# Kernel optimization log

Hardware: AMD Instinct MI355X
Metric: run time of the kernel (lower is better)

The kernel has to match this reference:

```python
import jax, jax.numpy as jnp
import numpy as np

TEMPERATURE = 0.5   # cfg.LOSS.TEMPERATURE
REG = 0.5           # Sinkhorn entropic regularization
NUM_ITER = 100      # numItermax in forward call
STOP_THR = 1e-9

BS, NUM_CLASSES, DIM = 16384, 1000, 512


def _l2norm(x):
    return x / jnp.linalg.norm(x, axis=-1, keepdims=True)


def setup_inputs() -> dict:
    key = jax.random.key(0)
    k1, k2, k3 = jax.random.split(key, 3)
    features = _l2norm(jax.random.normal(k1, (BS, DIM), jnp.float32))
    text_features = _l2norm(jax.random.normal(k2, (NUM_CLASSES, DIM), jnp.float32))
    ratios = jax.random.uniform(k3, (NUM_CLASSES,), jnp.float32)
    ratios = ratios / ratios.sum()  # class prior, sums to 1
    return {"features": features, "text_features": text_features, "ratios": ratios}


def sinkhorn_knopp(a, b, M, reg):
    """Faithful Sinkhorn-Knopp: u/v scaling loop with NaN/Inf bail-out and
    every-10-iters convergence check, unrolled as a masked lax.scan."""
    dim_a, dim_b = a.shape[0], b.shape[0]
    K = jnp.exp(M / -reg)                 # [dim_a, dim_b]
    Kp = (1.0 / a)[:, None] * K           # [dim_a, dim_b]
    u0 = jnp.ones((dim_a,), M.dtype) / dim_a
    v0 = jnp.ones((dim_b,), M.dtype) / dim_b

    def step(carry, ii):
        u, v, done = carry
        KtU = K.T @ u                     # [dim_b]
        v_new = b / KtU
        u_new = 1.0 / (Kp @ v_new)        # [dim_a]
        bad = (jnp.any(KtU == 0)
               | jnp.any(~jnp.isfinite(u_new))
               | jnp.any(~jnp.isfinite(v_new)))
        # err check (original does it when ii % 10 == 0)
        tmp2 = (u_new @ K) * v_new        # einsum('i,ij,j->j', u, K, v)
        err = jnp.linalg.norm(tmp2 - b)
        converged = ((ii % 10) == 0) & (err < STOP_THR)
        keep_prev = done | bad            # revert to uprev/vprev on bad, freeze after done
        u2 = jnp.where(keep_prev, u, u_new)
        v2 = jnp.where(keep_prev, v, v_new)
        return (u2, v2, done | bad | converged), None

    (u, v, _), _ = jax.lax.scan(step, (u0, v0, jnp.array(False)), jnp.arange(NUM_ITER))
    return u[:, None] * K * v[None, :]


def reference(features, text_features, ratios):
    sim_matrix = (features @ text_features.T) / TEMPERATURE   # [bs, C]
    cost_matrix = 1.0 - sim_matrix
    bs = features.shape[0]
    a = jnp.ones((bs,), features.dtype)       # row marginal (uniform over batch)
    b = ratios * bs                            # column marginal (class ratios)
    plan = sinkhorn_knopp(a, b, sim_matrix / cost_matrix, REG)  # [bs, C]
    return plan
```

## Files before the change

kernel.cpp:

```cpp
#include <hip/hip_runtime.h>
#include <hip/hip_bf16.h>

typedef float   f32x4_t  __attribute__((ext_vector_type(4)));
typedef float   f32x2_t  __attribute__((ext_vector_type(2)));
typedef __bf16  bf16x8_t __attribute__((ext_vector_type(8)));
typedef int     i32x4_t  __attribute__((ext_vector_type(4)));

#define N_ROWS   16384
#define N_COLS   1000
#define N_COLS_P 1024
#define N_DIM    512
#define N_ITER   100
#define PBLK     256
#define PTHR     512
#define NRED     64

__device__ __forceinline__ float ldf_sc1(const float* p) {
    return __hip_atomic_load(p, __ATOMIC_RELAXED, __HIP_MEMORY_SCOPE_AGENT);
}
__device__ __forceinline__ void stf_sc1(float* p, float v) {
    __hip_atomic_store(p, v, __ATOMIC_RELAXED, __HIP_MEMORY_SCOPE_AGENT);
}
__device__ __forceinline__ int ldi_sc1(const int* p) {
    return __hip_atomic_load(p, __ATOMIC_RELAXED, __HIP_MEMORY_SCOPE_AGENT);
}
__device__ __forceinline__ void sti_sc1(int* p, int v) {
    __hip_atomic_store(p, v, __ATOMIC_RELAXED, __HIP_MEMORY_SCOPE_AGENT);
}
__device__ __forceinline__ void st2_sc1(float* p, float a, float b) {
    const unsigned long long u =
        ((unsigned long long)__builtin_bit_cast(unsigned, b) << 32) |
        __builtin_bit_cast(unsigned, a);
    __hip_atomic_store((unsigned long long*)p, u, __ATOMIC_RELAXED,
                       __HIP_MEMORY_SCOPE_AGENT);
}
__device__ __forceinline__ void drain_vmem() {
    asm volatile("s_waitcnt vmcnt(0)" ::: "memory");
}

__device__ __forceinline__ unsigned short f2bf(float f) {
    unsigned int u = __builtin_bit_cast(unsigned int, f);
    u += 0x7FFFu + ((u >> 16) & 1u);
    return (unsigned short)(u >> 16);
}

template <int MODE>
__launch_bounds__(256)
__global__ void k_gemm(const float* __restrict__ F, const float* __restrict__ T,
                       void* __restrict__ Kout, float* __restrict__ cpart,
                       const float* __restrict__ v_com, const float* __restrict__ u_both,
                       const int* __restrict__ flags)
{
    __shared__ unsigned short lA[128 * 72];
    __shared__ unsigned short lB[128 * 72];
    __shared__ float cs_lds[4 * 64];

    const int bm = blockIdx.x;
    const int bn = blockIdx.y;
    const int m0 = bm << 7;
    const int n0 = bn << 7;
    const int t  = threadIdx.x;
    const int lane = t & 63;
    const int wid  = t >> 6;
    const int wr = wid >> 1;
    const int wc = wid & 1;

    f32x4_t acc[4][4];
#pragma unroll
    for (int a = 0; a < 4; ++a)
#pragma unroll
        for (int b = 0; b < 4; ++b)
            acc[a][b] = (f32x4_t){0.f, 0.f, 0.f, 0.f};

    const int srow = t >> 4;
    const int scol = (t & 15) << 2;

    for (int kt = 0; kt < N_DIM; kt += 64) {
#pragma unroll
        for (int r = 0; r < 8; ++r) {
            const int rr = srow + (r << 4);
            const float4 av = *(const float4*)(F + (size_t)(m0 + rr) * N_DIM + kt + scol);
            ushort4 a4; a4.x = f2bf(av.x); a4.y = f2bf(av.y); a4.z = f2bf(av.z); a4.w = f2bf(av.w);
            *(ushort4*)(&lA[rr * 72 + scol]) = a4;
            const int gn = n0 + rr;
            float4 bv = make_float4(0.f, 0.f, 0.f, 0.f);
            if (gn < N_COLS) bv = *(const float4*)(T + (size_t)gn * N_DIM + kt + scol);
            ushort4 b4; b4.x = f2bf(bv.x); b4.y = f2bf(bv.y); b4.z = f2bf(bv.z); b4.w = f2bf(bv.w);
            *(ushort4*)(&lB[rr * 72 + scol]) = b4;
        }
        __syncthreads();
#pragma unroll
        for (int ks = 0; ks < 2; ++ks) {
            bf16x8_t afr[4], bfr[4];
#pragma unroll
            for (int mf = 0; mf < 4; ++mf) {
                const int r = (wr << 6) + (mf << 4) + (lane & 15);
                const int off = r * 72 + (ks << 5) + ((lane >> 4) << 3);
                afr[mf] = __builtin_bit_cast(bf16x8_t, *(const i32x4_t*)(&lA[off]));
            }
#pragma unroll
            for (int nf = 0; nf < 4; ++nf) {
                const int r = (wc << 6) + (nf << 4) + (lane & 15);
                const int off = r * 72 + (ks << 5) + ((lane >> 4) << 3);
                bfr[nf] = __builtin_bit_cast(bf16x8_t, *(const i32x4_t*)(&lB[off]));
            }
#pragma unroll
            for (int mf = 0; mf < 4; ++mf)
#pragma unroll
                for (int nf = 0; nf < 4; ++nf)
                    acc[mf][nf] = __builtin_amdgcn_mfma_f32_16x16x32_bf16(
                        afr[mf], bfr[nf], acc[mf][nf], 0, 0, 0);
        }
        __syncthreads();
    }

    int usel = 2;
    if (MODE == 1) usel = flags[1];
    float csum[4] = {0.f, 0.f, 0.f, 0.f};
#pragma unroll
    for (int mf = 0; mf < 4; ++mf) {
#pragma unroll
        for (int nf = 0; nf < 4; ++nf) {
#pragma unroll
            for (int j = 0; j < 4; ++j) {
                const float d = acc[mf][nf][j];
                const float s = 2.f * d;
                const float M = s / (1.f - s);
                const float kv = __expf(-2.f * M);
                const int grow = m0 + (wr << 6) + (mf << 4) + ((lane >> 4) << 2) + j;
                const int gcol = n0 + (wc << 6) + (nf << 4) + (lane & 15);
                if (MODE == 0) {
                    ((unsigned short*)Kout)[(size_t)grow * N_COLS_P + gcol] =
                        (gcol < N_COLS) ? f2bf(kv) : (unsigned short)0;
                    csum[nf] += kv;
                } else {
                    if (gcol < N_COLS) {
                        const float u = (usel == 2) ? (1.f / 16384.f)
                                                    : u_both[(size_t)usel * N_ROWS + grow];
                        ((float*)Kout)[(size_t)grow * N_COLS + gcol] = u * kv * v_com[gcol];
                    }
                }
            }
        }
    }
    if (MODE == 0) {
#pragma unroll
        for (int nf = 0; nf < 4; ++nf) {
            csum[nf] += __shfl_xor(csum[nf], 16);
            csum[nf] += __shfl_xor(csum[nf], 32);
        }
        if (lane < 16) {
#pragma unroll
            for (int nf = 0; nf < 4; ++nf)
                cs_lds[wid * 64 + (nf << 4) + lane] = csum[nf];
        }
        __syncthreads();
        if (t < 128) {
            const int cw = t >> 6;
            const int c6 = t & 63;
            cpart[(size_t)bm * N_COLS_P + n0 + t] =
                cs_lds[cw * 64 + c6] + cs_lds[(cw + 2) * 64 + c6];
        }
    }
}

__launch_bounds__(128)
__global__ void k_init(const float* __restrict__ cpart, float* __restrict__ ktu0,
                       float* __restrict__ vcom, int* __restrict__ flags,
                       int* __restrict__ pst, int* __restrict__ rcnt,
                       int* __restrict__ flags2)
{
    const int j = blockIdx.x * 128 + threadIdx.x;
    if (j < N_COLS) {
        float s = 0.f;
        for (int p = 0; p < 128; ++p) s += cpart[(size_t)p * N_COLS_P + j];
        ktu0[j] = s * (1.f / 16384.f);
        vcom[j] = 1.f / 1000.f;
    } else {
        ktu0[j] = 1.f;
        vcom[j] = 0.f;
    }
    for (int z = j; z < PBLK * 16; z += 1024) pst[z] = 0;
    if (j < 128) { rcnt[j] = 0; flags2[j] = 0; }
    if (j < 4)   flags[j] = (j == 1) ? 2 : 0;
}

__launch_bounds__(PTHR, 2)
__global__ void k_persist(const unsigned short* __restrict__ Kb,
                          const float* __restrict__ ratios,
                          float* __restrict__ ktu,
                          float* __restrict__ utmp,
                          float* __restrict__ vcom,
                          float* __restrict__ partials,
                          int* __restrict__ flags,
                          int* __restrict__ pst,
                          int* __restrict__ rcnt,
                          int* __restrict__ flags2)
{
    __shared__ float vbuf[2][N_COLS_P];
    __shared__ float wp[8][N_COLS_P];
    __shared__ float redw[8][16];
    __shared__ float rbc;
    __shared__ int ibc;
    const int t = threadIdx.x, lane = t & 63, wid = t >> 6, b = blockIdx.x;
    const int row0 = (b << 6) + (wid << 3);
    const bool isred = (b < NRED);

    unsigned kp[8][8];
#pragma unroll
    for (int r = 0; r < 8; ++r) {
        const unsigned* rp = (const unsigned*)(Kb + (size_t)(row0 + r) * N_COLS_P);
#pragma unroll
        for (int q = 0; q < 8; ++q) kp[r][q] = rp[(q << 6) + lane];
    }
    const float bj0 = (t < N_COLS) ? ratios[t] * 16384.f : 0.f;
    const float bj1 = (t + PTHR < N_COLS) ? ratios[t + PTHR] * 16384.f : 0.f;

    int usel = 2;

    for (int ii = 0; ii <= N_ITER; ++ii) {
        const int p = ii & 1;
        float kc0, kc1;

        if (ii > 0) {
            if (t == 0) {
                while (ldi_sc1(&rcnt[ii - 1]) < NRED) __builtin_amdgcn_s_sleep(1);
                ibc = ldi_sc1(&flags2[ii - 1]);
            }
            __syncthreads();
            if (ibc) break;
            usel = (ii - 1) & 1;
            kc0 = ldf_sc1(&ktu[(p << 10) + t]);
            kc1 = ldf_sc1(&ktu[(p << 10) + t + PTHR]);
            if (((ii - 1) % 10) == 0) {
                const float vo0 = vbuf[usel][t], vo1 = vbuf[usel][t + PTHR];
                const float d0 = (t < N_COLS) ? kc0 * vo0 - bj0 : 0.f;
                const float d1 = (t + PTHR < N_COLS) ? kc1 * vo1 - bj1 : 0.f;
                float e = d0 * d0 + d1 * d1;
#pragma unroll
                for (int sh = 1; sh <= 32; sh <<= 1) e += __shfl_xor(e, sh);
                if (lane == 0) redw[wid][0] = e;
                __syncthreads();
                if (t == 0) {
                    float s = 0.f;
#pragma unroll
                    for (int w = 0; w < 8; ++w) s += redw[w][0];
                    rbc = s;
                }
                __syncthreads();
                if (rbc < 1e-18f) break;
            }
            if (ii == N_ITER) break;
        } else {
            kc0 = ldf_sc1(&ktu[t]);
            kc1 = ldf_sc1(&ktu[t + PTHR]);
        }

        const float v0 = bj0 / kc0;
        const float v1 = bj1 / kc1;
        const int badv = (kc0 == 0.f) | (kc1 == 0.f) | (!isfinite(v0)) | (!isfinite(v1));
        vbuf[p][t] = v0;
        vbuf[p][t + PTHR] = v1;
        if (__syncthreads_or(badv)) break;

        float vr[16];
#pragma unroll
        for (int q = 0; q < 8; ++q) {
            const f32x2_t vv = *(const f32x2_t*)&vbuf[p][(q << 7) + (lane << 1)];
            vr[2*q] = vv[0]; vr[2*q+1] = vv[1];
        }
        float dots[8];
#pragma unroll
        for (int r = 0; r < 8; ++r) {
            float p0 = 0.f, p1 = 0.f, p2 = 0.f, p3 = 0.f;
#pragma unroll
            for (int q = 0; q < 8; ++q) {
                const unsigned u = kp[r][q];
                const float lo = __builtin_bit_cast(float, u << 16);
                const float hi = __builtin_bit_cast(float, u & 0xFFFF0000u);
                if (q & 1) { p2 = fmaf(lo, vr[2*q], p2); p3 = fmaf(hi, vr[2*q+1], p3); }
                else       { p0 = fmaf(lo, vr[2*q], p0); p1 = fmaf(hi, vr[2*q+1], p1); }
            }
            dots[r] = (p0 + p1) + (p2 + p3);
        }
#pragma unroll
        for (int s = 1; s <= 32; s <<= 1) {
#pragma unroll
            for (int r = 0; r < 8; ++r) dots[r] += __shfl_xor(dots[r], s);
        }
        float u8[8];
        int ubad = 0;
#pragma unroll
        for (int r = 0; r < 8; ++r) { u8[r] = 1.f / dots[r]; ubad |= !isfinite(u8[r]); }
        if (lane == 0) {
            float* uo = utmp + ((size_t)p << 14) + row0;
#pragma unroll
            for (int r = 0; r < 8; ++r) uo[r] = u8[r];
        }
        if (__any(ubad) && lane == 0)
            __hip_atomic_fetch_or(&flags2[ii], 1, __ATOMIC_RELAXED,
                                  __HIP_MEMORY_SCOPE_AGENT);

        float creg[16];
#pragma unroll
        for (int e = 0; e < 16; ++e) creg[e] = 0.f;
#pragma unroll
        for (int r = 0; r < 8; ++r) {
#pragma unroll
            for (int q = 0; q < 8; ++q) {
                const unsigned u = kp[r][q];
                const float lo = __builtin_bit_cast(float, u << 16);
                const float hi = __builtin_bit_cast(float, u & 0xFFFF0000u);
                creg[2*q]   = fmaf(lo, u8[r], creg[2*q]);
                creg[2*q+1] = fmaf(hi, u8[r], creg[2*q+1]);
            }
        }
#pragma unroll
        for (int q = 0; q < 8; ++q)
            *(f32x2_t*)&wp[wid][(q << 7) + (lane << 1)] = (f32x2_t){creg[2*q], creg[2*q+1]};
        __syncthreads();
        {
            const int j2 = t << 1;
            f32x2_t s2 = *(const f32x2_t*)&wp[0][j2];
#pragma unroll
            for (int w = 1; w < 8; ++w) {
                const f32x2_t x = *(const f32x2_t*)&wp[w][j2];
                s2[0] += x[0]; s2[1] += x[1];
            }
            st2_sc1(&partials[((size_t)b << 10) + j2], s2[0], s2[1]);
        }
        drain_vmem();
        __syncthreads();
        if (t == 0) sti_sc1(&pst[b << 4], ii + 1);

        if (isred) {
            {
                const int prod = (wid << 5) + (lane & 31);
                const int pidx = prod << 4;
                for (;;) {
                    const int ok = (lane < 32) ? (ldi_sc1(&pst[pidx]) >= ii + 1) : 1;
                    if (__all(ok)) break;
                    __builtin_amdgcn_s_sleep(2);
                }
            }
            const int col = (b << 4) + (lane & 15);
            const int r0 = (wid << 5) + (lane >> 4);
            float s = 0.f;
#pragma unroll
            for (int k = 0; k < 8; ++k)
                s += ldf_sc1(&partials[((size_t)(r0 + (k << 2)) << 10) + col]);
            s += __shfl_xor(s, 16);
            s += __shfl_xor(s, 32);
            if (lane < 16) redw[wid][lane] = s;
            __syncthreads();
            if (t < 16) {
                float s2 = 0.f;
#pragma unroll
                for (int w = 0; w < 8; ++w) s2 += redw[w][t];
                const int c = (b << 4) + t;
                stf_sc1(&ktu[(((ii + 1) & 1) << 10) + c], (c < N_COLS) ? s2 : 1.f);
            }
            drain_vmem();
            __syncthreads();
            if (t == 0)
                __hip_atomic_fetch_add(&rcnt[ii], 1, __ATOMIC_RELAXED,
                                       __HIP_MEMORY_SCOPE_AGENT);
        }
    }

    if (b == 0) {
        float vf0, vf1;
        if (usel == 2) { vf0 = 1.f / 1000.f; vf1 = 1.f / 1000.f; }
        else           { vf0 = vbuf[usel][t]; vf1 = vbuf[usel][t + PTHR]; }
        if (t < N_COLS) vcom[t] = vf0;
        if (t + PTHR < N_COLS) vcom[t + PTHR] = vf1;
        if (t == 0) flags[1] = usel;
    }
}

extern "C" void kernel_launch(void* const* d_in, const int* in_sizes, int n_in,
                              void* d_out, int out_size, void* d_ws, size_t ws_size,
                              hipStream_t stream)
{
    const float* F      = (const float*)d_in[0];
    const float* T      = (const float*)d_in[1];
    const float* ratios = (const float*)d_in[2];
    float* out = (float*)d_out;
    unsigned short* Kb = (unsigned short*)d_out;

    float* ws        = (float*)d_ws;
    float* partials  = ws;
    float* ktu       = partials + (size_t)PBLK * N_COLS_P;
    float* utmp      = ktu + 2 * N_COLS_P;
    float* vcom      = utmp + 2 * N_ROWS;
    int*   flags     = (int*)(vcom + N_COLS_P);
    int*   pst       = flags + 4;
    int*   rcnt      = pst + PBLK * 16;
    int*   flags2    = rcnt + 128;
    const size_t need_bytes = ((size_t)PBLK * N_COLS_P + 2 * N_COLS_P + 2 * N_ROWS +
                               N_COLS_P) * sizeof(float) +
                              (4 + PBLK * 16 + 128 + 128) * sizeof(int);
    if (ws_size < need_bytes) return;

    k_gemm<0><<<dim3(128, 8), 256, 0, stream>>>(F, T, Kb, partials, nullptr, nullptr, flags);
    k_init<<<8, 128, 0, stream>>>(partials, ktu, vcom, flags, pst, rcnt, flags2);
    k_persist<<<PBLK, PTHR, 0, stream>>>(Kb, ratios, ktu, utmp, vcom, partials,
                                         flags, pst, rcnt, flags2);
    k_gemm<1><<<dim3(128, 8), 256, 0, stream>>>(F, T, out, nullptr, vcom, utmp, flags);
}
```

Before: 2.133 ms.

## Replace per-block producer flags with atomic counters and vectorized coherent loads

Producer blocks now signal completion of their column partials by incrementing a single per-iteration counter, replacing the per-block status slots that reducer warps had to poll. Reducers poll that counter with one thread and then read partials with two coherent dwordx4 loads per lane plus a shuffle reduction, instead of eight scalar atomic loads. The ktu and v handling is remapped to contiguous column pairs so each thread uses a single 64-bit coherent load and store. The aim is to cut the cost of the inter-block barrier and of the cross-block reduction on every Sinkhorn iteration, at the cost of contention on one atomic counter and inline asm loads that wait for completion immediately.

```diff
diff --git a/kernel.cpp b/kernel.cpp
--- a/kernel.cpp
+++ b/kernel.cpp
@@ -15,24 +15,33 @@
 #define PTHR     512
 #define NRED     64
 
-__device__ __forceinline__ float ldf_sc1(const float* p) {
-    return __hip_atomic_load(p, __ATOMIC_RELAXED, __HIP_MEMORY_SCOPE_AGENT);
-}
-__device__ __forceinline__ void stf_sc1(float* p, float v) {
-    __hip_atomic_store(p, v, __ATOMIC_RELAXED, __HIP_MEMORY_SCOPE_AGENT);
-}
 __device__ __forceinline__ int ldi_sc1(const int* p) {
     return __hip_atomic_load(p, __ATOMIC_RELAXED, __HIP_MEMORY_SCOPE_AGENT);
 }
-__device__ __forceinline__ void sti_sc1(int* p, int v) {
-    __hip_atomic_store(p, v, __ATOMIC_RELAXED, __HIP_MEMORY_SCOPE_AGENT);
-}
-__device__ __forceinline__ void st2_sc1(float* p, float a, float b) {
-    const unsigned long long u =
-        ((unsigned long long)__builtin_bit_cast(unsigned, b) << 32) |
-        __builtin_bit_cast(unsigned, a);
-    __hip_atomic_store((unsigned long long*)p, u, __ATOMIC_RELAXED,
-                       __HIP_MEMORY_SCOPE_AGENT);
+__device__ __forceinline__ void addi_sc1(int* p) {
+    __hip_atomic_fetch_add(p, 1, __ATOMIC_RELAXED, __HIP_MEMORY_SCOPE_AGENT);
+}
+__device__ __forceinline__ f32x2_t ld2_coh(const float* p) {
+    f32x2_t v;
+    asm volatile("global_load_dwordx2 %0, %1, off sc0 sc1\n\t"
+                 "s_waitcnt vmcnt(0)"
+                 : "=&v"(v) : "v"(p) : "memory");
+    return v;
+}
+__device__ __forceinline__ void ld4x2_coh(const float* pA, const float* pB,
+                                          f32x4_t* a, f32x4_t* b) {
+    asm volatile("global_load_dwordx4 %0, %2, off sc0 sc1\n\t"
+                 "global_load_dwordx4 %1, %3, off sc0 sc1\n\t"
+                 "s_waitcnt vmcnt(0)"
+                 : "=&v"(*a), "=&v"(*b) : "v"(pA), "v"(pB) : "memory");
+}
+__device__ __forceinline__ void st2_coh(float* p, f32x2_t v) {
+    asm volatile("global_store_dwordx2 %0, %1, off sc0 sc1"
+                 :: "v"(p), "v"(v) : "memory");
+}
+__device__ __forceinline__ void st1_coh(float* p, float v) {
+    asm volatile("global_store_dword %0, %1, off sc0 sc1"
+                 :: "v"(p), "v"(v) : "memory");
 }
 __device__ __forceinline__ void drain_vmem() {
     asm volatile("s_waitcnt vmcnt(0)" ::: "memory");
@@ -167,7 +176,7 @@
 __launch_bounds__(128)
 __global__ void k_init(const float* __restrict__ cpart, float* __restrict__ ktu0,
                        float* __restrict__ vcom, int* __restrict__ flags,
-                       int* __restrict__ pst, int* __restrict__ rcnt,
+                       int* __restrict__ pcnt, int* __restrict__ rcnt,
                        int* __restrict__ flags2)
 {
     const int j = blockIdx.x * 128 + threadIdx.x;
@@ -180,9 +189,8 @@
         ktu0[j] = 1.f;
         vcom[j] = 0.f;
     }
-    for (int z = j; z < PBLK * 16; z += 1024) pst[z] = 0;
-    if (j < 128) { rcnt[j] = 0; flags2[j] = 0; }
-    if (j < 4)   flags[j] = (j == 1) ? 2 : 0;
+    for (int z = j; z < 2048; z += 1024) { pcnt[z] = 0; rcnt[z] = 0; flags2[z] = 0; }
+    if (j < 4) flags[j] = (j == 1) ? 2 : 0;
 }
 
 __launch_bounds__(PTHR, 2)
@@ -193,7 +201,7 @@
                           float* __restrict__ vcom,
                           float* __restrict__ partials,
                           int* __restrict__ flags,
-                          int* __restrict__ pst,
+                          int* __restrict__ pcnt,
                           int* __restrict__ rcnt,
                           int* __restrict__ flags2)
 {
@@ -204,6 +212,7 @@
     __shared__ int ibc;
     const int t = threadIdx.x, lane = t & 63, wid = t >> 6, b = blockIdx.x;
     const int row0 = (b << 6) + (wid << 3);
+    const int c2 = t << 1;
     const bool isred = (b < NRED);
 
     unsigned kp[8][8];
@@ -213,29 +222,29 @@
 #pragma unroll
         for (int q = 0; q < 8; ++q) kp[r][q] = rp[(q << 6) + lane];
     }
-    const float bj0 = (t < N_COLS) ? ratios[t] * 16384.f : 0.f;
-    const float bj1 = (t + PTHR < N_COLS) ? ratios[t + PTHR] * 16384.f : 0.f;
+    const float bj0 = (c2 < N_COLS) ? ratios[c2] * 16384.f : 0.f;
+    const float bj1 = (c2 + 1 < N_COLS) ? ratios[c2 + 1] * 16384.f : 0.f;
 
     int usel = 2;
 
     for (int ii = 0; ii <= N_ITER; ++ii) {
         const int p = ii & 1;
-        float kc0, kc1;
+        f32x2_t kc;
 
         if (ii > 0) {
             if (t == 0) {
-                while (ldi_sc1(&rcnt[ii - 1]) < NRED) __builtin_amdgcn_s_sleep(1);
-                ibc = ldi_sc1(&flags2[ii - 1]);
+                while (ldi_sc1(&rcnt[(ii - 1) << 4]) < NRED)
+                    __builtin_amdgcn_s_sleep(1);
+                ibc = ldi_sc1(&flags2[(ii - 1) << 4]);
             }
             __syncthreads();
             if (ibc) break;
             usel = (ii - 1) & 1;
-            kc0 = ldf_sc1(&ktu[(p << 10) + t]);
-            kc1 = ldf_sc1(&ktu[(p << 10) + t + PTHR]);
+            kc = ld2_coh(&ktu[(p << 10) + c2]);
             if (((ii - 1) % 10) == 0) {
-                const float vo0 = vbuf[usel][t], vo1 = vbuf[usel][t + PTHR];
-                const float d0 = (t < N_COLS) ? kc0 * vo0 - bj0 : 0.f;
-                const float d1 = (t + PTHR < N_COLS) ? kc1 * vo1 - bj1 : 0.f;
+                const float vo0 = vbuf[usel][c2], vo1 = vbuf[usel][c2 + 1];
+                const float d0 = (c2 < N_COLS) ? kc[0] * vo0 - bj0 : 0.f;
+                const float d1 = (c2 + 1 < N_COLS) ? kc[1] * vo1 - bj1 : 0.f;
                 float e = d0 * d0 + d1 * d1;
 #pragma unroll
                 for (int sh = 1; sh <= 32; sh <<= 1) e += __shfl_xor(e, sh);
@@ -252,15 +261,14 @@
             }
             if (ii == N_ITER) break;
         } else {
-            kc0 = ldf_sc1(&ktu[t]);
-            kc1 = ldf_sc1(&ktu[t + PTHR]);
-        }
-
-        const float v0 = bj0 / kc0;
-        const float v1 = bj1 / kc1;
-        const int badv = (kc0 == 0.f) | (kc1 == 0.f) | (!isfinite(v0)) | (!isfinite(v1));
-        vbuf[p][t] = v0;
-        vbuf[p][t + PTHR] = v1;
+            kc = ld2_coh(&ktu[c2]);
+        }
+
+        const float v0 = bj0 / kc[0];
+        const float v1 = bj1 / kc[1];
+        const int badv = (kc[0] == 0.f) | (kc[1] == 0.f) |
+                         (!isfinite(v0)) | (!isfinite(v1));
+        *(f32x2_t*)&vbuf[p][c2] = (f32x2_t){v0, v1};
         if (__syncthreads_or(badv)) break;
 
         float vr[16];
@@ -298,7 +306,7 @@
             for (int r = 0; r < 8; ++r) uo[r] = u8[r];
         }
         if (__any(ubad) && lane == 0)
-            __hip_atomic_fetch_or(&flags2[ii], 1, __ATOMIC_RELAXED,
+            __hip_atomic_fetch_or(&flags2[ii << 4], 1, __ATOMIC_RELAXED,
                                   __HIP_MEMORY_SCOPE_AGENT);
 
         float creg[16];
@@ -327,53 +335,51 @@
                 const f32x2_t x = *(const f32x2_t*)&wp[w][j2];
                 s2[0] += x[0]; s2[1] += x[1];
             }
-            st2_sc1(&partials[((size_t)b << 10) + j2], s2[0], s2[1]);
+            st2_coh(&partials[((size_t)b << 10) + j2], s2);
         }
         drain_vmem();
         __syncthreads();
-        if (t == 0) sti_sc1(&pst[b << 4], ii + 1);
+        if (t == 0) addi_sc1(&pcnt[ii << 4]);
 
         if (isred) {
-            {
-                const int prod = (wid << 5) + (lane & 31);
-                const int pidx = prod << 4;
-                for (;;) {
-                    const int ok = (lane < 32) ? (ldi_sc1(&pst[pidx]) >= ii + 1) : 1;
-                    if (__all(ok)) break;
-                    __builtin_amdgcn_s_sleep(2);
-                }
-            }
-            const int col = (b << 4) + (lane & 15);
-            const int r0 = (wid << 5) + (lane >> 4);
-            float s = 0.f;
-#pragma unroll
-            for (int k = 0; k < 8; ++k)
-                s += ldf_sc1(&partials[((size_t)(r0 + (k << 2)) << 10) + col]);
-            s += __shfl_xor(s, 16);
-            s += __shfl_xor(s, 32);
-            if (lane < 16) redw[wid][lane] = s;
+            if (t == 0) {
+                while (ldi_sc1(&pcnt[ii << 4]) < PBLK)
+                    __builtin_amdgcn_s_sleep(1);
+            }
+            __syncthreads();
+            const int cbase = (b << 4) + ((lane & 3) << 2);
+            const int rowA  = (wid << 4) + (lane >> 2);
+            f32x4_t a, bq;
+            ld4x2_coh(&partials[((size_t)rowA << 10) + cbase],
+                      &partials[((size_t)(rowA + 128) << 10) + cbase], &a, &bq);
+            f32x4_t s4;
+#pragma unroll
+            for (int e = 0; e < 4; ++e) s4[e] = a[e] + bq[e];
+#pragma unroll
+            for (int sh = 4; sh <= 32; sh <<= 1) {
+#pragma unroll
+                for (int e = 0; e < 4; ++e) s4[e] += __shfl_xor(s4[e], sh);
+            }
+            if (lane < 4) *(f32x4_t*)&redw[wid][lane << 2] = s4;
             __syncthreads();
             if (t < 16) {
                 float s2 = 0.f;
 #pragma unroll
                 for (int w = 0; w < 8; ++w) s2 += redw[w][t];
                 const int c = (b << 4) + t;
-                stf_sc1(&ktu[(((ii + 1) & 1) << 10) + c], (c < N_COLS) ? s2 : 1.f);
+                st1_coh(&ktu[(((ii + 1) & 1) << 10) + c], (c < N_COLS) ? s2 : 1.f);
             }
             drain_vmem();
             __syncthreads();
-            if (t == 0)
-                __hip_atomic_fetch_add(&rcnt[ii], 1, __ATOMIC_RELAXED,
-                                       __HIP_MEMORY_SCOPE_AGENT);
+            if (t == 0) addi_sc1(&rcnt[ii << 4]);
         }
     }
 
     if (b == 0) {
-        float vf0, vf1;
-        if (usel == 2) { vf0 = 1.f / 1000.f; vf1 = 1.f / 1000.f; }
-        else           { vf0 = vbuf[usel][t]; vf1 = vbuf[usel][t + PTHR]; }
-        if (t < N_COLS) vcom[t] = vf0;
-        if (t + PTHR < N_COLS) vcom[t + PTHR] = vf1;
+        if (c2 < N_COLS)
+            vcom[c2] = (usel == 2) ? (1.f / 1000.f) : vbuf[usel][c2];
+        if (c2 + 1 < N_COLS)
+            vcom[c2 + 1] = (usel == 2) ? (1.f / 1000.f) : vbuf[usel][c2 + 1];
         if (t == 0) flags[1] = usel;
     }
 }
@@ -394,17 +400,17 @@
     float* utmp      = ktu + 2 * N_COLS_P;
     float* vcom      = utmp + 2 * N_ROWS;
     int*   flags     = (int*)(vcom + N_COLS_P);
-    int*   pst       = flags + 4;
-    int*   rcnt      = pst + PBLK * 16;
-    int*   flags2    = rcnt + 128;
+    int*   pcnt      = flags + 16;
+    int*   rcnt      = pcnt + 2048;
+    int*   flags2    = rcnt + 2048;
     const size_t need_bytes = ((size_t)PBLK * N_COLS_P + 2 * N_COLS_P + 2 * N_ROWS +
                                N_COLS_P) * sizeof(float) +
-                              (4 + PBLK * 16 + 128 + 128) * sizeof(int);
+                              (16 + 3 * 2048) * sizeof(int);
     if (ws_size < need_bytes) return;
 
     k_gemm<0><<<dim3(128, 8), 256, 0, stream>>>(F, T, Kb, partials, nullptr, nullptr, flags);
-    k_init<<<8, 128, 0, stream>>>(partials, ktu, vcom, flags, pst, rcnt, flags2);
+    k_init<<<8, 128, 0, stream>>>(partials, ktu, vcom, flags, pcnt, rcnt, flags2);
     k_persist<<<PBLK, PTHR, 0, stream>>>(Kb, ratios, ktu, utmp, vcom, partials,
-                                         flags, pst, rcnt, flags2);
+                                         flags, pcnt, rcnt, flags2);
     k_gemm<1><<<dim3(128, 8), 256, 0, stream>>>(F, T, out, nullptr, vcom, utmp, flags);
 }
```

Measured after the change: 2.235 ms. 4.8% more time.
